# Performance work log

Measured on AMD Instinct MI355X. Metric: run time of the kernel, lower is better.

The kernel has to match this reference:

```python
import jax, jax.numpy as jnp
import numpy as np

B, IMG, P, CIN = 4, 384, 16, 3
G = IMG // P            # 24 patches per side
NP = G * G              # 576 patch tokens
N = NP + 1              # +cls
D, H, L, MLP, NC = 768, 12, 12, 3072, 1000
HD = D // H
SCALE = HD ** -0.5
NUM_REL = (2 * G - 1) * (2 * G - 1) + 3   # (2*1-1)*(2G-1)*(2G-1)+3 = 2212
EPS = 1e-6


def gen_rel_index():
    # window (1, G, G): depth diff is always 0, reduces to 2D BEiT indexing
    coords = np.stack(np.meshgrid(np.arange(G), np.arange(G), indexing='ij')).reshape(2, -1)
    rel = (coords[:, :, None] - coords[:, None, :]).transpose(1, 2, 0).copy()  # (NP,NP,2)
    rel[:, :, 0] += G - 1
    rel[:, :, 1] += G - 1
    rel[:, :, 0] *= 2 * G - 1
    idx = np.zeros((N, N), dtype=np.int32)
    idx[1:, 1:] = rel.sum(-1)
    idx[0, :] = NUM_REL - 3
    idx[:, 0] = NUM_REL - 2
    idx[0, 0] = NUM_REL - 1
    return jnp.asarray(idx)


def setup_inputs() -> dict:
    key = jax.random.key(0)
    ks = jax.random.split(key, 20)
    s = 0.02
    inp = {
        'x': jax.random.normal(ks[0], (B, CIN, IMG, IMG), jnp.float32),
        'patch_w': s * jax.random.normal(ks[1], (D, CIN * P * P), jnp.float32),
        'patch_b': jnp.zeros((D,), jnp.float32),
        'cls_token': s * jax.random.normal(ks[2], (1, 1, D), jnp.float32),
        'pos_embed': s * jax.random.normal(ks[3], (1, N, D), jnp.float32),
        'ln1_w': jnp.ones((L, D), jnp.float32),
        'ln1_b': jnp.zeros((L, D), jnp.float32),
        'qkv_w': s * jax.random.normal(ks[4], (L, 3 * D, D), jnp.float32),
        'q_bias': jnp.zeros((L, D), jnp.float32),
        'v_bias': jnp.zeros((L, D), jnp.float32),
        'proj_w': s * jax.random.normal(ks[5], (L, D, D), jnp.float32),
        'proj_b': jnp.zeros((L, D), jnp.float32),
        'ln2_w': jnp.ones((L, D), jnp.float32),
        'ln2_b': jnp.zeros((L, D), jnp.float32),
        'fc1_w': s * jax.random.normal(ks[6], (L, MLP, D), jnp.float32),
        'fc1_b': jnp.zeros((L, MLP), jnp.float32),
        'fc2_w': s * jax.random.normal(ks[7], (L, D, MLP), jnp.float32),
        'fc2_b': jnp.zeros((L, D), jnp.float32),
        'rel_table': s * jax.random.normal(ks[8], (L, NUM_REL, H), jnp.float32),
        'fc_norm_w': jnp.ones((D,), jnp.float32),
        'fc_norm_b': jnp.zeros((D,), jnp.float32),
        'head_w': s * jax.random.normal(ks[9], (NC, D), jnp.float32),
        'head_b': jnp.zeros((NC,), jnp.float32),
        'rel_index': gen_rel_index(),
    }
    return inp


def _ln(x, w, b):
    m = x.mean(-1, keepdims=True)
    v = ((x - m) ** 2).mean(-1, keepdims=True)
    return (x - m) * jax.lax.rsqrt(v + EPS) * w + b


def _beit_fwd(x, patch_w, patch_b, cls_token, pos_embed,
              ln1_w, ln1_b, qkv_w, q_bias, v_bias, proj_w, proj_b,
              ln2_w, ln2_b, fc1_w, fc1_b, fc2_w, fc2_b, rel_table,
              fc_norm_w, fc_norm_b, head_w, head_b, rel_index):
    # patch embed: conv P x P stride P == reshape + matmul; patch vec order (c, ph, pw)
    patches = x.reshape(B, CIN, G, P, G, P).transpose(0, 2, 4, 1, 3, 5).reshape(B, NP, CIN * P * P)
    tok = patches @ patch_w.T + patch_b                      # (B, NP, D)
    h = jnp.concatenate([jnp.broadcast_to(cls_token, (B, 1, D)), tok], axis=1) + pos_embed

    def block(h, p):
        l1w, l1b, qw, qb, vb, pw, pb, l2w, l2b, f1w, f1b, f2w, f2b, rt = p
        y = _ln(h, l1w, l1b)
        bias = jnp.concatenate([qb, jnp.zeros_like(qb), vb])  # k_bias frozen zeros
        qkv = (y @ qw.T + bias).reshape(B, N, 3, H, HD).transpose(2, 0, 3, 1, 4)
        q, k, v = qkv[0] * SCALE, qkv[1], qkv[2]              # (B,H,N,HD)
        attn = jnp.einsum('bhnd,bhmd->bhnm', q, k)
        rel = rt[rel_index].transpose(2, 0, 1)                # (H,N,N)
        attn = jax.nn.softmax(attn + rel[None], axis=-1)
        o = jnp.einsum('bhnm,bhmd->bhnd', attn, v).transpose(0, 2, 1, 3).reshape(B, N, D)
        h = h + (o @ pw.T + pb)
        y = _ln(h, l2w, l2b)
        y = jax.nn.gelu(y @ f1w.T + f1b, approximate=False) @ f2w.T + f2b
        return h + y, None

    xs = (ln1_w, ln1_b, qkv_w, q_bias, v_bias, proj_w, proj_b,
          ln2_w, ln2_b, fc1_w, fc1_b, fc2_w, fc2_b, rel_table)
    h, _ = jax.lax.scan(block, h, xs)

    pooled = h[:, 1:].mean(axis=1)                            # global_pool='avg' drops cls
    return _ln(pooled, fc_norm_w, fc_norm_b) @ head_w.T + head_b  # (B, NC)


def reference(x, patch_w, patch_b, cls_token, pos_embed,
              ln1_w, ln1_b, qkv_w, q_bias, v_bias, proj_w, proj_b,
              ln2_w, ln2_b, fc1_w, fc1_b, fc2_w, fc2_b, rel_table,
              fc_norm_w, fc_norm_b, head_w, head_b, rel_index):
    return _beit_fwd(x, patch_w, patch_b, cls_token, pos_embed,
                     ln1_w, ln1_b, qkv_w, q_bias, v_bias, proj_w, proj_b,
                     ln2_w, ln2_b, fc1_w, fc1_b, fc2_w, fc2_b, rel_table,
                     fc_norm_w, fc_norm_b, head_w, head_b, rel_index)
```

## Files before the change

### kernel.cpp

```cpp
#include <hip/hip_runtime.h>
#include <math.h>

typedef unsigned short u16;
typedef __bf16 bf16x8_t __attribute__((ext_vector_type(8)));
typedef u16 u16x8 __attribute__((ext_vector_type(8)));
typedef float f32x4 __attribute__((ext_vector_type(4)));

#define CBATCH 4
#define CN 577
#define CNP 576
#define CD 768
#define CH 12
#define CHD 64
#define CL 12
#define CMLP 3072
#define CVP 640
#define CROWS (CBATCH*CN)
#define CROWSP 2432
#define CNN2 332929
#define CBH (CBATCH*CH)
#define CSKP 2
#define CSKF 4
#define CMT 37

__device__ __forceinline__ float b2f(u16 u){
  unsigned x = ((unsigned)u) << 16;
  return __builtin_bit_cast(float, x);
}
__device__ __forceinline__ u16 f2b(float f){
  unsigned x = __builtin_bit_cast(unsigned, f);
  unsigned r = x + 0x7fffu + ((x >> 16) & 1u);
  return (u16)(r >> 16);
}

__device__ __forceinline__ f32x4 MFMA(u16x8 a, u16x8 b, f32x4 c){
  return __builtin_amdgcn_mfma_f32_16x16x32_bf16(
      __builtin_bit_cast(bf16x8_t, a), __builtin_bit_cast(bf16x8_t, b), c, 0, 0, 0);
}

__device__ __forceinline__ void gl_lds16(const u16* g, u16* l){
  __builtin_amdgcn_global_load_lds(
      (const __attribute__((address_space(1))) unsigned int*)g,
      (__attribute__((address_space(3))) unsigned int*)l, 16, 0, 0);
}

__device__ __forceinline__ int xcd_chunk(int o, int nwg){
  int q8 = nwg >> 3, r8 = nwg & 7;
  int xcd = o & 7, sl = o >> 3;
  return (xcd < r8 ? xcd*(q8+1) : r8*(q8+1) + (xcd - r8)*q8) + sl;
}


__global__ void cvt_kernel(const float* __restrict__ src, u16* __restrict__ dst, int n){
  int i = (blockIdx.x * 256 + threadIdx.x) * 4;
  if(i < n){
    float4 v = *reinterpret_cast<const float4*>(src + i);
    ushort4 o;
    o.x = f2b(v.x); o.y = f2b(v.y); o.z = f2b(v.z); o.w = f2b(v.w);
    *reinterpret_cast<ushort4*>(dst + i) = o;
  }
}

__global__ void zero_kernel(u16* __restrict__ p, int n){
  int i = (blockIdx.x * 256 + threadIdx.x) * 8;
  if(i < n){
    u16x8 z = {0,0,0,0,0,0,0,0};
    *reinterpret_cast<u16x8*>(p + i) = z;
  }
}

__global__ void im2col_kernel(const float* __restrict__ x, u16* __restrict__ out){
  int id = blockIdx.x * 256 + threadIdx.x;
  if(id >= 2304*768) return;
  int col = id % 768, row = id / 768;
  int b = row / 576, p = row % 576;
  int gy = p / 24, gx = p % 24;
  int c = col >> 8, rem = col & 255, py = rem >> 4, px = rem & 15;
  float v = x[(((long)(b*3 + c)*384) + gy*16 + py)*384 + gx*16 + px];
  out[id] = f2b(v);
}

__global__ void clspos_kernel(const float* __restrict__ cls, const float* __restrict__ pos,
                              float* __restrict__ h){
  int id = blockIdx.x * 256 + threadIdx.x;
  if(id < CBATCH*CD){
    int b = id / CD, d = id % CD;
    h[(long)b*CN*CD + d] = cls[d] + pos[d];
  }
}

template<bool BF16OUT>
__global__ void ln_kernel(const float* __restrict__ x, const float* __restrict__ w,
                          const float* __restrict__ bsh, u16* __restrict__ yb,
                          float* __restrict__ yf){
  int r = blockIdx.x;
  int tid = threadIdx.x;
  const float* px = x + (long)r*CD;
  float v0 = px[tid], v1 = px[tid+256], v2 = px[tid+512];
  __shared__ float red[4];
  float s = v0 + v1 + v2;
  #pragma unroll
  for(int m=1;m<64;m<<=1) s += __shfl_xor(s, m);
  if((tid & 63) == 0) red[tid>>6] = s;
  __syncthreads();
  s = red[0]+red[1]+red[2]+red[3];
  float mean = s * (1.0f/768.0f);
  float d0 = v0-mean, d1 = v1-mean, d2 = v2-mean;
  float s2 = d0*d0 + d1*d1 + d2*d2;
  __syncthreads();
  #pragma unroll
  for(int m=1;m<64;m<<=1) s2 += __shfl_xor(s2, m);
  if((tid & 63) == 0) red[tid>>6] = s2;
  __syncthreads();
  s2 = red[0]+red[1]+red[2]+red[3];
  float rs = rsqrtf(s2*(1.0f/768.0f) + 1e-6f);
  float o0 = d0*rs*w[tid]     + bsh[tid];
  float o1 = d1*rs*w[tid+256] + bsh[tid+256];
  float o2 = d2*rs*w[tid+512] + bsh[tid+512];
  if(BF16OUT){
    yb[(long)r*CD + tid]     = f2b(o0);
    yb[(long)r*CD + tid+256] = f2b(o1);
    yb[(long)r*CD + tid+512] = f2b(o2);
  } else {
    yf[(long)r*CD + tid]     = o0;
    yf[(long)r*CD + tid+256] = o1;
    yf[(long)r*CD + tid+512] = o2;
  }
}

template<bool DOLN, int NSK>
__global__ void resid_ln_kernel(float* __restrict__ h, const float* __restrict__ part,
    const float* __restrict__ bias, const float* __restrict__ w,
    const float* __restrict__ bsh, u16* __restrict__ y){
  int r = blockIdx.x, tid = threadIdx.x;
  float v[3];
  #pragma unroll
  for(int j=0;j<3;j++){
    int c = tid + j*256;
    float t = h[(long)r*CD + c] + bias[c];
    #pragma unroll
    for(int sk=0; sk<NSK; sk++) t += part[((long)sk*CROWS + r)*CD + c];
    v[j] = t;
    h[(long)r*CD + c] = t;
  }
  if constexpr(DOLN){
    __shared__ float red[4];
    float s = v[0]+v[1]+v[2];
    #pragma unroll
    for(int m=1;m<64;m<<=1) s += __shfl_xor(s, m);
    if((tid & 63) == 0) red[tid>>6] = s;
    __syncthreads();
    s = red[0]+red[1]+red[2]+red[3];
    float mean = s * (1.0f/768.0f);
    float d0=v[0]-mean, d1=v[1]-mean, d2=v[2]-mean;
    float s2 = d0*d0+d1*d1+d2*d2;
    __syncthreads();
    #pragma unroll
    for(int m=1;m<64;m<<=1) s2 += __shfl_xor(s2, m);
    if((tid & 63) == 0) red[tid>>6] = s2;
    __syncthreads();
    s2 = red[0]+red[1]+red[2]+red[3];
    float rs = rsqrtf(s2*(1.0f/768.0f) + 1e-6f);
    y[(long)r*CD + tid]     = f2b(d0*rs*w[tid]     + bsh[tid]);
    y[(long)r*CD + tid+256] = f2b(d1*rs*w[tid+256] + bsh[tid+256]);
    y[(long)r*CD + tid+512] = f2b(d2*rs*w[tid+512] + bsh[tid+512]);
  }
}

__global__ void relbias_all_kernel(const int* __restrict__ ridx, const float* __restrict__ rtab,
                                   u16* __restrict__ attb){
  int id = blockIdx.x * 256 + threadIdx.x;
  if(id >= CNN2) return;
  int l = blockIdx.y;
  int idx = ridx[id];
  const float* rowp = rtab + (long)l*2212*12 + (long)idx*12;
  u16* dst = attb + (long)l*12*CNN2;
  #pragma unroll
  for(int hh=0; hh<12; hh++)
    dst[(long)hh*CNN2 + id] = f2b(rowp[hh]);
}

__global__ __launch_bounds__(256) void attn_kernel(
    const u16* __restrict__ q, const u16* __restrict__ k,
    const u16* __restrict__ vt, const u16* __restrict__ attb,
    u16* __restrict__ o_){
  __shared__ __align__(16) u16 lK[2][64*64];
  __shared__ __align__(16) u16 lV[2][64*64];
  __shared__ u16 pt[4][16*72];
  const int tid = threadIdx.x, lane = tid & 63, wv = tid >> 6;
  const int i15 = lane & 15, g4 = lane >> 4;
  const int o = blockIdx.y * 10 + blockIdx.x;
  const int cm = xcd_chunk(o, 480);
  const int bh = cm / 10, qt = cm % 10;
  const int b = bh / CH, hh = bh % CH;
  const int qrow0 = qt*64 + wv*16;
  const u16* qp = q + ((long)bh*CN + qrow0 + i15)*CHD + g4*8;
  u16x8 qa0 = *reinterpret_cast<const u16x8*>(qp);
  u16x8 qa1 = *reinterpret_cast<const u16x8*>(qp + 32);
  const u16* kbase = k + (long)bh*CN*CHD;
  const u16* vbase = vt + (long)bh*CHD*CVP;
  const u16* bb = attb + (long)hh*CNN2;

  const int srow = wv*16 + (lane>>3);
  const int scol = (lane&7)*8;
  const int sdst = wv*16*64;

  f32x4 po[4];
  float m[4], l[4];
  #pragma unroll
  for(int i=0;i<4;i++){ po[i]=(f32x4){0,0,0,0}; m[i]=-3.0e38f; l[i]=0.0f; }

  auto STAGE = [&](int t, int buf){
    const int kv0 = t*64;
    const u16* ks = kbase + ((long)(kv0 + srow))*CHD + scol;
    const u16* vs = vbase + ((long)srow)*CVP + kv0 + scol;
    gl_lds16(ks,          &lK[buf][sdst]);
    gl_lds16(ks + 8*CHD,  &lK[buf][sdst + 8*64]);
    gl_lds16(vs,          &lV[buf][sdst]);
    gl_lds16(vs + 8*CVP,  &lV[buf][sdst + 8*64]);
  };

  STAGE(0, 0);
  for(int t=0;t<10;t++){
    if(t+1 < 10){
      STAGE(t+1, (t+1)&1);
      asm volatile("s_waitcnt vmcnt(4)" ::: "memory");
    } else {
      asm volatile("s_waitcnt vmcnt(0)" ::: "memory");
    }
    __syncthreads();
    const int buf = t&1;
    const int kv0 = t*64;
    f32x4 sa[4];
    #pragma unroll
    for(int fc=0;fc<4;fc++){
      u16x8 k0 = *reinterpret_cast<const u16x8*>(&lK[buf][(fc*16+i15)*64 + g4*8]);
      u16x8 k1 = *reinterpret_cast<const u16x8*>(&lK[buf][(fc*16+i15)*64 + 32 + g4*8]);
      f32x4 z = (f32x4){0,0,0,0};
      z = MFMA(qa0, k0, z);
      z = MFMA(qa1, k1, z);
      sa[fc] = z;
    }
    float s[4][4];
    #pragma unroll
    for(int fc=0;fc<4;fc++){
      int kvc = kv0 + fc*16 + i15;
      bool valid = kvc < CN;
      #pragma unroll
      for(int r=0;r<4;r++){
        int qr = qrow0 + g4*4 + r;
        float bias = b2f(bb[(long)qr*CN + kvc]);
        s[fc][r] = valid ? (sa[fc][r] + bias) : -1e30f;
      }
    }
    float tm[4], ts[4], sc[4];
    #pragma unroll
    for(int r=0;r<4;r++)
      tm[r] = fmaxf(fmaxf(s[0][r],s[1][r]), fmaxf(s[2][r],s[3][r]));
    #pragma unroll
    for(int msk=1; msk<16; msk<<=1)
      #pragma unroll
      for(int r=0;r<4;r++)
        tm[r] = fmaxf(tm[r], __shfl_xor(tm[r], msk));
    #pragma unroll
    for(int r=0;r<4;r++){
      float mn = fmaxf(m[r], tm[r]);
      sc[r] = exp2f((m[r]-mn)*1.4426950408889634f);
      m[r] = mn;
      ts[r] = 0.f;
    }
    #pragma unroll
    for(int fc=0;fc<4;fc++)
      #pragma unroll
      for(int r=0;r<4;r++){
        float p = exp2f((s[fc][r]-m[r])*1.4426950408889634f);
        s[fc][r] = p; ts[r] += p;
      }
    #pragma unroll
    for(int msk=1; msk<16; msk<<=1)
      #pragma unroll
      for(int r=0;r<4;r++)
        ts[r] += __shfl_xor(ts[r], msk);
    #pragma unroll
    for(int r=0;r<4;r++) l[r] = l[r]*sc[r] + ts[r];
    #pragma unroll
    for(int d=0; d<4; d++)
      #pragma unroll
      for(int r=0;r<4;r++) po[d][r] *= sc[r];
    #pragma unroll
    for(int fc=0;fc<4;fc++)
      #pragma unroll
      for(int r=0;r<4;r++)
        pt[wv][(g4*4+r)*72 + fc*16 + i15] = f2b(s[fc][r]);
    u16x8 pa0 = *reinterpret_cast<const u16x8*>(&pt[wv][i15*72 + g4*8]);
    u16x8 pa1 = *reinterpret_cast<const u16x8*>(&pt[wv][i15*72 + 32 + g4*8]);
    #pragma unroll
    for(int d=0; d<4; d++){
      u16x8 v0 = *reinterpret_cast<const u16x8*>(&lV[buf][(d*16+i15)*64 + g4*8]);
      u16x8 v1 = *reinterpret_cast<const u16x8*>(&lV[buf][(d*16+i15)*64 + 32 + g4*8]);
      po[d] = MFMA(pa0, v0, po[d]);
      po[d] = MFMA(pa1, v1, po[d]);
    }
    __syncthreads();
  }
  #pragma unroll
  for(int d=0; d<4; d++)
    #pragma unroll
    for(int r=0;r<4;r++){
      int qr = qrow0 + g4*4 + r;
      if(qr < CN)
        o_[((long)(b*CN + qr))*CD + hh*CHD + d*16 + i15] = f2b(po[d][r] / l[r]);
    }
}

__global__ void pool_kernel(const float* __restrict__ h, float* __restrict__ pooled){
  int id = blockIdx.x * 256 + threadIdx.x;
  if(id >= CBATCH*CD) return;
  int b = id / CD, d = id % CD;
  const float* p = h + ((long)b*CN + 1)*CD + d;
  float s = 0.0f;
  for(int i=0;i<CNP;i++) s += p[(long)i*CD];
  pooled[id] = s * (1.0f/576.0f);
}

__global__ void head_kernel(const float* __restrict__ xn, const float* __restrict__ hw,
                            const float* __restrict__ hb, float* __restrict__ out){
  int nc = blockIdx.x;
  int tid = threadIdx.x;
  const float* wr = hw + (long)nc*CD;
  float w0 = wr[tid], w1 = wr[tid+256], w2 = wr[tid+512];
  __shared__ float red[4];
  for(int b=0;b<CBATCH;b++){
    const float* xr = xn + (long)b*CD;
    float s = w0*xr[tid] + w1*xr[tid+256] + w2*xr[tid+512];
    #pragma unroll
    for(int m=1;m<64;m<<=1) s += __shfl_xor(s, m);
    if((tid&63)==0) red[tid>>6] = s;
    __syncthreads();
    if(tid==0) out[b*1000 + nc] = red[0]+red[1]+red[2]+red[3] + hb[nc];
    __syncthreads();
  }
}


struct EpiArgs {
  float* hres;
  u16* outb;
  const float* bias;
  const float* pos;
  const float* qb;
  const float* vb;
  u16* q;
  u16* k;
  u16* vt;
  float* part;
};

enum { EPI_PATCH=0, EPI_QKV, EPI_GELU, EPI_PART };

template<int EPI>
__global__ __launch_bounds__(256,4) void gemm4(const u16* __restrict__ A, const u16* __restrict__ Bm,
    int M, int N, int K, int lda, int ldb, EpiArgs e){
  __shared__ __align__(16) u16 lA[3][64*32];
  __shared__ __align__(16) u16 lB[3][128*32];
  const int tid  = threadIdx.x;
  const int lane = tid & 63;
  const int wv   = tid >> 6;

  const int gx = gridDim.x, gy = gridDim.y;
  const int o = blockIdx.y * gx + blockIdx.x;
  const int cm = xcd_chunk(o, gx*gy);
  const int bn = (cm / gy) * 128;
  const int bm = (cm % gy) * 64;

  const int z  = blockIdx.z;
  A  += (long)z * K;
  Bm += (long)z * K;

  const int srow = wv*16 + (lane>>2);
  const u16* Asb = A  + (long)(bm + srow)*lda + (lane&3)*8;
  const u16* Bsb = Bm + (long)(bn + srow)*ldb + (lane&3)*8;
  const int ldst = wv*16*32;

  const int rbase = (wv>>1)*32;
  const int cbase = (wv&1)*64;
  const int i15 = lane & 15;
  const int k8off = (lane>>4)<<3;

  f32x4 acc[2][4];
  #pragma unroll
  for(int i=0;i<2;i++)
    #pragma unroll
    for(int j=0;j<4;j++)
      acc[i][j] = (f32x4){0.0f,0.0f,0.0f,0.0f};

  const int nkt = K >> 5;

  auto STAGE = [&](int kt, int slot){
    const u16* Ak = Asb + (long)kt*32;
    const u16* Bk = Bsb + (long)kt*32;
    gl_lds16(Ak,          &lA[slot][ldst]);
    gl_lds16(Bk,          &lB[slot][ldst]);
    gl_lds16(Bk + 64*ldb, &lB[slot][ldst + 64*32]);
  };

  STAGE(0, 0);
  if(nkt > 1) STAGE(1, 1);

  for(int kt=0; kt<nkt; kt++){
    if(kt+1 < nkt) asm volatile("s_waitcnt vmcnt(3) lgkmcnt(0)" ::: "memory");
    else           asm volatile("s_waitcnt vmcnt(0) lgkmcnt(0)" ::: "memory");
    __builtin_amdgcn_s_barrier();
    int nxt2 = kt + 2;
    if(nxt2 < nkt){ int sl = nxt2 % 3; STAGE(nxt2, sl); }
    const int cur = kt % 3;
    u16x8 af[2], bfr[4];
    #pragma unroll
    for(int f=0; f<2; f++)
      af[f]  = *reinterpret_cast<const u16x8*>(&lA[cur][(rbase + f*16 + i15)*32 + k8off]);
    #pragma unroll
    for(int f=0; f<4; f++)
      bfr[f] = *reinterpret_cast<const u16x8*>(&lB[cur][(cbase + f*16 + i15)*32 + k8off]);
    #pragma unroll
    for(int fr=0; fr<2; fr++)
      #pragma unroll
      for(int fc=0; fc<4; fc++)
        acc[fr][fc] = MFMA(af[fr], bfr[fc], acc[fr][fc]);
  }

  #pragma unroll
  for(int fr=0; fr<2; fr++){
    #pragma unroll
    for(int fc=0; fc<4; fc++){
      #pragma unroll
      for(int r=0;r<4;r++){
        int row = bm + rbase + fr*16 + ((lane>>4)<<2) + r;
        int col = bn + cbase + fc*16 + i15;
        if(row >= M || col >= N) continue;
        float v = acc[fr][fc][r];
        if constexpr(EPI == EPI_PATCH){
          int b = row/576, p = row%576;
          e.hres[((long)b*CN + 1 + p)*CD + col] = v + e.bias[col] + e.pos[(long)(1+p)*CD + col];
        } else if constexpr(EPI == EPI_QKV){
          int b = row/CN, n = row%CN;
          if(col < 768){
            int hh = col>>6, d = col&63;
            e.q[(((long)(b*CH+hh))*CN + n)*CHD + d] = f2b((v + e.qb[col]) * 0.125f);
          } else if(col < 1536){
            int c2 = col-768; int hh = c2>>6, d = c2&63;
            e.k[(((long)(b*CH+hh))*CN + n)*CHD + d] = f2b(v);
          } else {
            int c2 = col-1536; int hh = c2>>6, d = c2&63;
            e.vt[(((long)(b*CH+hh))*CHD + d)*CVP + n] = f2b(v + e.vb[c2]);
          }
        } else if constexpr(EPI == EPI_GELU){
          float t = v + e.bias[col];
          e.outb[(long)row*N + col] = f2b(t * 0.5f * (1.0f + erff(t*0.70710678118f)));
        } else {
          e.part[((long)z*CROWS + row)*CD + col] = v;
        }
      }
    }
  }
}


extern "C" void kernel_launch(void* const* d_in, const int* in_sizes, int n_in,
                              void* d_out, int out_size, void* d_ws, size_t ws_size,
                              hipStream_t stream){
  const float* x        = (const float*)d_in[0];
  const float* patch_w  = (const float*)d_in[1];
  const float* patch_b  = (const float*)d_in[2];
  const float* cls_tok  = (const float*)d_in[3];
  const float* pos_emb  = (const float*)d_in[4];
  const float* ln1_w    = (const float*)d_in[5];
  const float* ln1_b    = (const float*)d_in[6];
  const float* qkv_w    = (const float*)d_in[7];
  const float* q_bias   = (const float*)d_in[8];
  const float* v_bias   = (const float*)d_in[9];
  const float* proj_w   = (const float*)d_in[10];
  const float* proj_b   = (const float*)d_in[11];
  const float* ln2_w    = (const float*)d_in[12];
  const float* ln2_b    = (const float*)d_in[13];
  const float* fc1_w    = (const float*)d_in[14];
  const float* fc1_b    = (const float*)d_in[15];
  const float* fc2_w    = (const float*)d_in[16];
  const float* fc2_b    = (const float*)d_in[17];
  const float* rel_tab  = (const float*)d_in[18];
  const float* fcn_w    = (const float*)d_in[19];
  const float* fcn_b    = (const float*)d_in[20];
  const float* head_w   = (const float*)d_in[21];
  const float* head_b   = (const float*)d_in[22];
  const int*   rel_idx  = (const int*)d_in[23];
  float* out = (float*)d_out;
  char* ws = (char*)d_ws;

  size_t off = 0;
  auto alloc = [&](size_t bytes)->size_t{
    size_t o = off; off += (bytes + 255) & ~(size_t)255; return o;
  };
  const size_t OFF_H    = alloc((size_t)CROWS*CD*4);
  const size_t OFF_Y    = alloc((size_t)CROWSP*CD*2);
  const size_t OFF_Q    = alloc(((size_t)CBH*CN + 128)*CHD*2);
  const size_t OFF_K    = alloc(((size_t)CBH*CN + 128)*CHD*2);
  const size_t OFF_VT   = alloc((size_t)CBH*CHD*CVP*2);
  const size_t OFF_O    = alloc((size_t)CROWSP*CD*2);
  const size_t OFF_HID  = alloc((size_t)CROWSP*CMLP*2);
  const size_t OFF_PART = alloc((size_t)CSKF*CROWS*CD*4);
  const size_t OFF_ATTB = alloc(((size_t)CL*CH*CNN2 + 64*1024)*2);
  const size_t OFF_WP0  = alloc((size_t)768*768*2);
  const size_t OFF_WQA  = alloc((size_t)CL*2304*768*2);
  const size_t OFF_WPA  = alloc((size_t)CL*768*768*2);
  const size_t OFF_W1A  = alloc((size_t)CL*3072*768*2);
  const size_t OFF_W2A  = alloc((size_t)CL*768*3072*2);
  const size_t OFF_PL   = alloc((size_t)CBATCH*CD*4);
  const size_t OFF_NM   = alloc((size_t)CBATCH*CD*4);
  (void)ws_size; (void)in_sizes; (void)n_in; (void)out_size;

  float* h      = (float*)(ws + OFF_H);
  u16*   y      = (u16*)(ws + OFF_Y);
  u16*   qb_    = (u16*)(ws + OFF_Q);
  u16*   kb_    = (u16*)(ws + OFF_K);
  u16*   vt_    = (u16*)(ws + OFF_VT);
  u16*   o_     = (u16*)(ws + OFF_O);
  u16*   hid    = (u16*)(ws + OFF_HID);
  float* part   = (float*)(ws + OFF_PART);
  u16*   attb   = (u16*)(ws + OFF_ATTB);
  u16*   wp0    = (u16*)(ws + OFF_WP0);
  u16*   wqA    = (u16*)(ws + OFF_WQA);
  u16*   wpA    = (u16*)(ws + OFF_WPA);
  u16*   w1A    = (u16*)(ws + OFF_W1A);
  u16*   w2A    = (u16*)(ws + OFF_W2A);
  float* pooled = (float*)(ws + OFF_PL);
  float* normed = (float*)(ws + OFF_NM);

  auto cvt = [&](const float* src, u16* dst, long n){
    cvt_kernel<<<dim3((unsigned)((n/4 + 255)/256)), dim3(256), 0, stream>>>(src, dst, (int)n);
  };

  {
    int n = CBH*CHD*CVP;
    zero_kernel<<<dim3((n/8 + 255)/256), dim3(256), 0, stream>>>(vt_, n);
  }
  im2col_kernel<<<dim3((2304*768 + 255)/256), dim3(256), 0, stream>>>(x, hid);
  cvt(patch_w, wp0, 768*768);
  cvt(qkv_w,  wqA, (long)CL*2304*768);
  cvt(proj_w, wpA, (long)CL*768*768);
  cvt(fc1_w,  w1A, (long)CL*3072*768);
  cvt(fc2_w,  w2A, (long)CL*768*3072);
  relbias_all_kernel<<<dim3((CNN2 + 255)/256, CL), dim3(256), 0, stream>>>(
      rel_idx, rel_tab, attb);

  {
    EpiArgs e{}; e.hres = h; e.bias = patch_b; e.pos = pos_emb;
    gemm4<EPI_PATCH><<<dim3(6,36,1), dim3(256), 0, stream>>>(
        hid, wp0, 2304, 768, 768, 768, 768, e);
  }
  clspos_kernel<<<dim3(12), dim3(256), 0, stream>>>(cls_tok, pos_emb, h);

  ln_kernel<true><<<dim3(CROWS), dim3(256), 0, stream>>>(
      h, ln1_w, ln1_b, y, nullptr);

  for(int l=0; l<CL; l++){
    {
      EpiArgs e{}; e.qb = q_bias + l*CD; e.vb = v_bias + l*CD;
      e.q = qb_; e.k = kb_; e.vt = vt_;
      gemm4<EPI_QKV><<<dim3(18,CMT,1), dim3(256), 0, stream>>>(
          y, wqA + (long)l*2304*768, CROWS, 2304, 768, 768, 768, e);
    }
    attn_kernel<<<dim3(10, CBH), dim3(256), 0, stream>>>(
        qb_, kb_, vt_, attb + (long)l*CH*CNN2, o_);
    {
      EpiArgs e{}; e.part = part;
      gemm4<EPI_PART><<<dim3(6,CMT,CSKP), dim3(256), 0, stream>>>(
          o_, wpA + (long)l*768*768, CROWS, 768, 768/CSKP, 768, 768, e);
    }
    resid_ln_kernel<true,CSKP><<<dim3(CROWS), dim3(256), 0, stream>>>(
        h, part, proj_b + l*CD, ln2_w + l*CD, ln2_b + l*CD, y);
    {
      EpiArgs e{}; e.outb = hid; e.bias = fc1_b + l*CMLP;
      gemm4<EPI_GELU><<<dim3(24,CMT,1), dim3(256), 0, stream>>>(
          y, w1A + (long)l*3072*768, CROWS, 3072, 768, 768, 768, e);
    }
    {
      EpiArgs e{}; e.part = part;
      gemm4<EPI_PART><<<dim3(6,CMT,CSKF), dim3(256), 0, stream>>>(
          hid, w2A + (long)l*768*3072, CROWS, 768, 3072/CSKF, 3072, 3072, e);
    }
    if(l+1 < CL){
      resid_ln_kernel<true,CSKF><<<dim3(CROWS), dim3(256), 0, stream>>>(
          h, part, fc2_b + l*CD, ln1_w + (l+1)*CD, ln1_b + (l+1)*CD, y);
    } else {
      resid_ln_kernel<false,CSKF><<<dim3(CROWS), dim3(256), 0, stream>>>(
          h, part, fc2_b + l*CD, nullptr, nullptr, nullptr);
    }
  }

  pool_kernel<<<dim3(12), dim3(256), 0, stream>>>(h, pooled);
  ln_kernel<false><<<dim3(CBATCH), dim3(256), 0, stream>>>(
      pooled, fcn_w, fcn_b, nullptr, normed);
  head_kernel<<<dim3(1000), dim3(256), 0, stream>>>(normed, head_w, head_b, out);
}
```

Before: 2.087 ms.

## Gather relative position bias in attention from LDS table instead of materialized bias

```diff
diff --git a/kernel.cpp b/kernel.cpp
--- a/kernel.cpp
+++ b/kernel.cpp
@@ -22,6 +22,7 @@
 #define CSKP 2
 #define CSKF 4
 #define CMT 37
+#define CRTP 2304
 
 __device__ __forceinline__ float b2f(u16 u){
   unsigned x = ((unsigned)u) << 16;
@@ -167,26 +168,27 @@
   }
 }
 
-__global__ void relbias_all_kernel(const int* __restrict__ ridx, const float* __restrict__ rtab,
-                                   u16* __restrict__ attb){
-  int id = blockIdx.x * 256 + threadIdx.x;
-  if(id >= CNN2) return;
+__global__ void rtT_kernel(const float* __restrict__ rtab, u16* __restrict__ rtT){
+  int rel = blockIdx.x * 256 + threadIdx.x;
   int l = blockIdx.y;
-  int idx = ridx[id];
-  const float* rowp = rtab + (long)l*2212*12 + (long)idx*12;
-  u16* dst = attb + (long)l*12*CNN2;
-  #pragma unroll
-  for(int hh=0; hh<12; hh++)
-    dst[(long)hh*CNN2 + id] = f2b(rowp[hh]);
+  if(rel >= CRTP) return;
+  const float* row = rtab + ((long)l*2212 + rel)*12;
+  #pragma unroll
+  for(int hh=0; hh<12; hh++){
+    u16 v = 0;
+    if(rel < 2212) v = f2b(row[hh]);
+    rtT[((long)l*12 + hh)*CRTP + rel] = v;
+  }
 }
 
 __global__ __launch_bounds__(256) void attn_kernel(
     const u16* __restrict__ q, const u16* __restrict__ k,
-    const u16* __restrict__ vt, const u16* __restrict__ attb,
-    u16* __restrict__ o_){
+    const u16* __restrict__ vt, const int* __restrict__ ridx,
+    const u16* __restrict__ rtT, u16* __restrict__ o_){
   __shared__ __align__(16) u16 lK[2][64*64];
   __shared__ __align__(16) u16 lV[2][64*64];
   __shared__ u16 pt[4][16*72];
+  __shared__ __align__(16) u16 rtc[CRTP];
   const int tid = threadIdx.x, lane = tid & 63, wv = tid >> 6;
   const int i15 = lane & 15, g4 = lane >> 4;
   const int o = blockIdx.y * 10 + blockIdx.x;
@@ -199,7 +201,16 @@
   u16x8 qa1 = *reinterpret_cast<const u16x8*>(qp + 32);
   const u16* kbase = k + (long)bh*CN*CHD;
   const u16* vbase = vt + (long)bh*CHD*CVP;
-  const u16* bb = attb + (long)hh*CNN2;
+
+  {
+    const u16* rc = rtT + (long)hh*CRTP;
+    #pragma unroll
+    for(int i=0;i<CRTP/(256*8); i++)
+      ;
+    for(int i = tid; i < CRTP/8; i += 256)
+      *reinterpret_cast<u16x8*>(&rtc[i*8]) = *reinterpret_cast<const u16x8*>(rc + i*8);
+  }
+  __syncthreads();
 
   const int srow = wv*16 + (lane>>3);
   const int scol = (lane&7)*8;
@@ -222,15 +233,25 @@
 
   STAGE(0, 0);
   for(int t=0;t<10;t++){
+    const int kv0 = t*64;
+    int idxr[4][4];
+    #pragma unroll
+    for(int fc=0;fc<4;fc++){
+      int kvc = kv0 + fc*16 + i15; if(kvc > 576) kvc = 576;
+      #pragma unroll
+      for(int r=0;r<4;r++){
+        int qr = qrow0 + g4*4 + r; if(qr > 576) qr = 576;
+        idxr[fc][r] = ridx[qr*CN + kvc];
+      }
+    }
     if(t+1 < 10){
       STAGE(t+1, (t+1)&1);
-      asm volatile("s_waitcnt vmcnt(4)" ::: "memory");
+      asm volatile("s_waitcnt vmcnt(4) lgkmcnt(0)" ::: "memory");
     } else {
-      asm volatile("s_waitcnt vmcnt(0)" ::: "memory");
-    }
-    __syncthreads();
+      asm volatile("s_waitcnt vmcnt(0) lgkmcnt(0)" ::: "memory");
+    }
+    __builtin_amdgcn_s_barrier();
     const int buf = t&1;
-    const int kv0 = t*64;
     f32x4 sa[4];
     #pragma unroll
     for(int fc=0;fc<4;fc++){
@@ -248,8 +269,7 @@
       bool valid = kvc < CN;
       #pragma unroll
       for(int r=0;r<4;r++){
-        int qr = qrow0 + g4*4 + r;
-        float bias = b2f(bb[(long)qr*CN + kvc]);
+        float bias = b2f(rtc[idxr[fc][r]]);
         s[fc][r] = valid ? (sa[fc][r] + bias) : -1e30f;
       }
     }
@@ -301,7 +321,7 @@
       po[d] = MFMA(pa0, v0, po[d]);
       po[d] = MFMA(pa1, v1, po[d]);
     }
-    __syncthreads();
+    __builtin_amdgcn_s_barrier();
   }
   #pragma unroll
   for(int d=0; d<4; d++)
@@ -506,8 +526,8 @@
   const size_t OFF_VT   = alloc((size_t)CBH*CHD*CVP*2);
   const size_t OFF_O    = alloc((size_t)CROWSP*CD*2);
   const size_t OFF_HID  = alloc((size_t)CROWSP*CMLP*2);
-  const size_t OFF_PART = alloc((size_t)CSKF*CROWS*CD*4);
-  const size_t OFF_ATTB = alloc(((size_t)CL*CH*CNN2 + 64*1024)*2);
+  const size_t OFF_PART = alloc((size_t)4*CROWS*CD*4);
+  const size_t OFF_RTT  = alloc((size_t)CL*12*CRTP*2);
   const size_t OFF_WP0  = alloc((size_t)768*768*2);
   const size_t OFF_WQA  = alloc((size_t)CL*2304*768*2);
   const size_t OFF_WPA  = alloc((size_t)CL*768*768*2);
@@ -525,7 +545,7 @@
   u16*   o_     = (u16*)(ws + OFF_O);
   u16*   hid    = (u16*)(ws + OFF_HID);
   float* part   = (float*)(ws + OFF_PART);
-  u16*   attb   = (u16*)(ws + OFF_ATTB);
+  u16*   rtT    = (u16*)(ws + OFF_RTT);
   u16*   wp0    = (u16*)(ws + OFF_WP0);
   u16*   wqA    = (u16*)(ws + OFF_WQA);
   u16*   wpA    = (u16*)(ws + OFF_WPA);
@@ -548,8 +568,7 @@
   cvt(proj_w, wpA, (long)CL*768*768);
   cvt(fc1_w,  w1A, (long)CL*3072*768);
   cvt(fc2_w,  w2A, (long)CL*768*3072);
-  relbias_all_kernel<<<dim3((CNN2 + 255)/256, CL), dim3(256), 0, stream>>>(
-      rel_idx, rel_tab, attb);
+  rtT_kernel<<<dim3(CRTP/256, CL), dim3(256), 0, stream>>>(rel_tab, rtT);
 
   {
     EpiArgs e{}; e.hres = h; e.bias = patch_b; e.pos = pos_emb;
@@ -569,7 +588,7 @@
           y, wqA + (long)l*2304*768, CROWS, 2304, 768, 768, 768, e);
     }
     attn_kernel<<<dim3(10, CBH), dim3(256), 0, stream>>>(
-        qb_, kb_, vt_, attb + (long)l*CH*CNN2, o_);
+        qb_, kb_, vt_, rel_idx, rtT + (long)l*12*CRTP, o_);
     {
       EpiArgs e{}; e.part = part;
       gemm4<EPI_PART><<<dim3(6,CMT,CSKP), dim3(256), 0, stream>>>(
```

Result: no change. 2.082 ms (-0.2%).
